# Performance work log

Measured on AMD Instinct MI355X. Metric: run time of the kernel, lower is better.

The kernel has to match this reference:

```python
import jax, jax.numpy as jnp
import numpy as np

EMBED_DIM = 1024
NUM_HEADS = 16
HEAD_DIM = EMBED_DIM // NUM_HEADS


def setup_inputs() -> dict:
    key = jax.random.key(0)
    ks = jax.random.split(key, 5)
    T, B, E = 2048, 2, EMBED_DIM
    s = 1.0 / np.sqrt(E)
    return {
        "x": jax.random.normal(ks[0], (T, B, E), jnp.float32),
        "wq": jax.random.normal(ks[1], (E, E), jnp.float32) * s,
        "bq": jnp.zeros((E,), jnp.float32),
        "wk": jax.random.normal(ks[2], (E, E), jnp.float32) * s,
        "bk": jnp.zeros((E,), jnp.float32),
        "wv": jax.random.normal(ks[3], (E, E), jnp.float32) * s,
        "bv": jnp.zeros((E,), jnp.float32),
        "wo": jax.random.normal(ks[4], (E, E), jnp.float32) * s,
        "bo": jnp.zeros((E,), jnp.float32),
    }


def reference(x, wq, bq, wk, bk, wv, bv, wo, bo):
    # x: [T, B, E] (Time x Batch x Channel), self-attention: query = key = value = x
    T, B, E = x.shape
    H, D = NUM_HEADS, HEAD_DIM
    scaling = D ** -0.5
    # Linear projections (torch Linear: y = x @ W.T + b)
    q = (jnp.einsum('tbe,fe->tbf', x, wq) + bq) * scaling
    k = jnp.einsum('tbe,fe->tbf', x, wk) + bk
    v = jnp.einsum('tbe,fe->tbf', x, wv) + bv
    # reshape to [B*H, T, D] equivalent -> use [B, H, T, D]
    q = q.reshape(T, B, H, D).transpose(1, 2, 0, 3)  # [B,H,T,D]
    k = k.reshape(T, B, H, D).transpose(1, 2, 0, 3)
    v = v.reshape(T, B, H, D).transpose(1, 2, 0, 3)
    # scores: [B,H,T,S], fp32 softmax
    scores = jnp.einsum('bhtd,bhsd->bhts', q, k)
    probs = jax.nn.softmax(scores.astype(jnp.float32), axis=-1).astype(x.dtype)
    attn = jnp.einsum('bhts,bhsd->bhtd', probs, v)  # [B,H,T,D]
    attn = attn.transpose(2, 0, 1, 3).reshape(T, B, E)
    out = jnp.einsum('tbe,fe->tbf', attn, wo) + bo
    return out
```

## Files before the change

### kernel.cpp

```cpp
#include <hip/hip_runtime.h>
#include <cstddef>
#include <cstdint>

#define T_DIM 2048
#define E_DIM 1024
#define M_DIM 4096

typedef __attribute__((ext_vector_type(8))) short short8;
typedef __attribute__((ext_vector_type(8))) _Float16 half8;
typedef __attribute__((ext_vector_type(4))) _Float16 half4;
typedef __attribute__((ext_vector_type(4))) float f32x4;

__device__ __forceinline__ short f16_bits(float v) {
  return __builtin_bit_cast(short, (_Float16)v);
}
__device__ __forceinline__ unsigned int pk2(float a, float b) {
  return __builtin_bit_cast(unsigned int, __builtin_amdgcn_cvt_pkrtz(a, b));
}
__device__ __forceinline__ half8 h8(short8 s) { return __builtin_bit_cast(half8, s); }

__device__ __forceinline__ void gl_lds16(const short* g, const short* l) {
  __builtin_amdgcn_global_load_lds(
      (const __attribute__((address_space(1))) unsigned int*)g,
      (__attribute__((address_space(3))) unsigned int*)l, 16, 0, 0);
}

__global__ __launch_bounds__(256) void convert_all(
    const float* __restrict__ x, const float* __restrict__ wq,
    const float* __restrict__ wk, const float* __restrict__ wv,
    const float* __restrict__ wo,
    short* __restrict__ xh, short* __restrict__ wqh, short* __restrict__ wkh,
    short* __restrict__ wvh, short* __restrict__ woh)
{
  const int bid = blockIdx.x;
  const float* in; short* hi; int base;
  if (bid < 4096)      { in = x;  hi = xh;  base = 0;    }
  else if (bid < 5120) { in = wq; hi = wqh; base = 4096; }
  else if (bid < 6144) { in = wk; hi = wkh; base = 5120; }
  else if (bid < 7168) { in = wv; hi = wvh; base = 6144; }
  else                 { in = wo; hi = woh; base = 7168; }
  const int i = (bid - base) * 256 + threadIdx.x;
  float4 v = ((const float4*)in)[i];
  uint2 p;
  p.x = (unsigned short)f16_bits(v.x) | ((unsigned int)(unsigned short)f16_bits(v.y) << 16);
  p.y = (unsigned short)f16_bits(v.z) | ((unsigned int)(unsigned short)f16_bits(v.w) << 16);
  ((uint2*)hi)[i] = p;
}

__global__ __launch_bounds__(256) void gemm_qkv(
    const short* __restrict__ xh,
    const short* __restrict__ wqh, const short* __restrict__ wkh,
    const short* __restrict__ wvh,
    const float* __restrict__ bq, const float* __restrict__ bk,
    const float* __restrict__ bv,
    short* __restrict__ qo, short* __restrict__ ko, short* __restrict__ vto)
{
  __shared__ __align__(16) short smem[128 * 64 * 2];
  short* Ah = smem;
  short* Wh = smem + 8192;
  const int tid = threadIdx.x;
  const int lane = tid & 63;
  const int w = tid >> 6;
  const int quad = lane >> 4;
  const int l15 = lane & 15;
  const int sel = blockIdx.x >> 3;
  const int n0 = (blockIdx.x & 7) * 128;
  const int m0 = blockIdx.y * 128;

  const short* wsel = sel == 0 ? wqh : sel == 1 ? wkh : wvh;
  const float* bias = sel == 0 ? bq : sel == 1 ? bk : bv;
  const float scale = sel == 0 ? 0.125f * 1.44269504088896f : 1.0f;

  const short* gsrc = (w < 2) ? xh : wsel;
  short* lbuf = (w < 2) ? Ah : Wh;
  const int rbase = (w < 2) ? m0 : n0;
  const int lrow8 = lane >> 3;
  const int gph8 = lane & 7;
  const int kg = (gph8 - lrow8) & 7;

  f32x4 zero = {0.f, 0.f, 0.f, 0.f};
  f32x4 acc[4][4];
#pragma unroll
  for (int i = 0; i < 4; ++i)
#pragma unroll
    for (int j = 0; j < 4; ++j) acc[i][j] = zero;

  const int wm = w & 1, wn = w >> 1;

  for (int k0 = 0; k0 < E_DIM; k0 += 64) {
    __syncthreads();
#pragma unroll
    for (int jj = 0; jj < 8; ++jj) {
      int j = (w & 1) * 8 + jj;
      int r = j * 8 + lrow8;
      gl_lds16(gsrc + (size_t)(rbase + r) * E_DIM + k0 + kg * 8, lbuf + j * 512);
    }
    __syncthreads();
#pragma unroll
    for (int ks = 0; ks < 2; ++ks) {
      short8 ahf[4];
#pragma unroll
      for (int i = 0; i < 4; ++i) {
        int r = wm * 64 + i * 16 + l15;
        ahf[i] = *(const short8*)&Ah[r * 64 + ((ks * 4 + quad + r) & 7) * 8];
      }
#pragma unroll
      for (int j = 0; j < 4; ++j) {
        int r = wn * 64 + j * 16 + l15;
        short8 bhf = *(const short8*)&Wh[r * 64 + ((ks * 4 + quad + r) & 7) * 8];
#pragma unroll
        for (int i = 0; i < 4; ++i)
          acc[i][j] = __builtin_amdgcn_mfma_f32_16x16x32_f16(h8(ahf[i]), h8(bhf), acc[i][j], 0, 0, 0);
      }
    }
  }

  if (sel < 2) {
#pragma unroll
    for (int j = 0; j < 4; ++j) {
      const int gc = n0 + wn * 64 + j * 16 + l15;
      const float bb = bias[gc];
      const int h = gc >> 6, d = gc & 63;
      short* dst = sel == 0 ? qo : ko;
#pragma unroll
      for (int i = 0; i < 4; ++i)
#pragma unroll
        for (int reg = 0; reg < 4; ++reg) {
          const int gm = m0 + wm * 64 + i * 16 + quad * 4 + reg;
          const float val = (acc[i][j][reg] + bb) * scale;
          const int t = gm >> 1, b = gm & 1;
          dst[((size_t)(b * 16 + h) * T_DIM + t) * 64 + d] = f16_bits(val);
        }
    }
  } else {
    short* Tb = smem;
    const int by = blockIdx.y;
#pragma unroll
    for (int R = 0; R < 2; ++R) {
      __syncthreads();
      if (wn == R) {
#pragma unroll
        for (int j = 0; j < 4; ++j) {
          const int nl = j * 16 + l15;
          const int gc = n0 + R * 64 + nl;
          const float bb = bias[gc];
#pragma unroll
          for (int i = 0; i < 4; ++i) {
            const int tp = wm * 32 + i * 8 + quad * 2;
            unsigned int lo = pk2(acc[i][j][0] + bb, acc[i][j][2] + bb);
            unsigned int hi = pk2(acc[i][j][1] + bb, acc[i][j][3] + bb);
            const int g0 = tp >> 3;
            const int sub = tp & 7;
            *(unsigned int*)&Tb[nl * 128 + ((g0 + nl) & 15) * 8 + sub] = lo;
            *(unsigned int*)&Tb[nl * 128 + ((g0 + 8 + nl) & 15) * 8 + sub] = hi;
          }
        }
      }
      __syncthreads();
#pragma unroll
      for (int ii = 0; ii < 4; ++ii) {
        const int n = w * 16 + ii * 4 + quad;
        const int g = (l15 - n) & 15;
        short8 vvec = *(const short8*)&Tb[n * 128 + l15 * 8];
        const int gc = n0 + R * 64 + n;
        const int h = gc >> 6, d = gc & 63;
        const int b = g >> 3;
        const int t = by * 64 + (g & 7) * 8;
        *(short8*)&vto[((size_t)(b * 16 + h) * 64 + d) * T_DIM + t] = vvec;
      }
    }
  }
}

__global__ __launch_bounds__(512, 4) void gemm_out_fused(
    const short* __restrict__ attn, const short* __restrict__ woh,
    const float* __restrict__ bo, float* __restrict__ out)
{
  __shared__ __align__(16) short smem[32768];
  const int tid = threadIdx.x;
  const int lane = tid & 63;
  const int w = tid >> 6;
  const int g = w >> 2;
  const int wg = w & 3;
  const int quad = lane >> 4;
  const int l15 = lane & 15;
  const int n0 = blockIdx.x * 128;
  const int m0 = blockIdx.y * 128;

  short* Ah = smem + g * 16384;
  short* Wh = Ah + 8192;
  const short* gsrc = (wg < 2) ? attn : woh;
  short* lbuf = (wg < 2) ? Ah : Wh;
  const int rbase = (wg < 2) ? m0 : n0;
  const int lrow8 = lane >> 3;
  const int gph8 = lane & 7;
  const int kg = (gph8 - lrow8) & 7;

  f32x4 zero = {0.f, 0.f, 0.f, 0.f};
  f32x4 acc[4][4];
#pragma unroll
  for (int i = 0; i < 4; ++i)
#pragma unroll
    for (int j = 0; j < 4; ++j) acc[i][j] = zero;

  const int wm = wg & 1, wn = wg >> 1;

  for (int k0 = g * 512; k0 < g * 512 + 512; k0 += 64) {
    __syncthreads();
#pragma unroll
    for (int jj = 0; jj < 8; ++jj) {
      int j = (wg & 1) * 8 + jj;
      int r = j * 8 + lrow8;
      gl_lds16(gsrc + (size_t)(rbase + r) * E_DIM + k0 + kg * 8, lbuf + j * 512);
    }
    __syncthreads();
#pragma unroll
    for (int ks = 0; ks < 2; ++ks) {
      short8 ahf[4];
#pragma unroll
      for (int i = 0; i < 4; ++i) {
        int r = wm * 64 + i * 16 + l15;
        ahf[i] = *(const short8*)&Ah[r * 64 + ((ks * 4 + quad + r) & 7) * 8];
      }
#pragma unroll
      for (int j = 0; j < 4; ++j) {
        int r = wn * 64 + j * 16 + l15;
        short8 bhf = *(const short8*)&Wh[r * 64 + ((ks * 4 + quad + r) & 7) * 8];
#pragma unroll
        for (int i = 0; i < 4; ++i)
          acc[i][j] = __builtin_amdgcn_mfma_f32_16x16x32_f16(h8(ahf[i]), h8(bhf), acc[i][j], 0, 0, 0);
      }
    }
  }

  __syncthreads();
  f32x4* Osc = (f32x4*)smem;
  if (g == 1) {
    f32x4* dst = Osc + wg * 1024;
#pragma unroll
    for (int i = 0; i < 4; ++i)
#pragma unroll
      for (int j = 0; j < 4; ++j)
        dst[(i * 4 + j) * 64 + lane] = acc[i][j];
  }
  __syncthreads();
  if (g == 0) {
    f32x4* src = Osc + wg * 1024;
#pragma unroll
    for (int j = 0; j < 4; ++j) {
      const int gc = n0 + wn * 64 + j * 16 + l15;
      const float bb = bo[gc];
#pragma unroll
      for (int i = 0; i < 4; ++i) {
        f32x4 t = src[(i * 4 + j) * 64 + lane];
#pragma unroll
        for (int reg = 0; reg < 4; ++reg) {
          const int gm = m0 + wm * 64 + i * 16 + quad * 4 + reg;
          out[(size_t)gm * E_DIM + gc] = acc[i][j][reg] + t[reg] + bb;
        }
      }
    }
  }
}

__global__ __launch_bounds__(256, 2) void attn_mfma(
    const short* __restrict__ q, const short* __restrict__ k,
    const short* __restrict__ vt, short* __restrict__ attn)
{
  __shared__ __align__(16) short SMEM[32768];
  __shared__ float l_red[4][128];
  short* Qs = SMEM;
  short* KV = SMEM + 8192;

  const int tid = threadIdx.x;
  const int lane = tid & 63;
  const int w = tid >> 6;
  const int quad = lane >> 4;
  const int l15 = lane & 15;
  const int bhid = blockIdx.y;
  const int b = bhid >> 4, h = bhid & 15;
  const int t0 = blockIdx.x * 128;

  const short* qb = q + (size_t)bhid * T_DIM * 64;
  const short* kb = k + (size_t)bhid * T_DIM * 64;
  const short* vb = vt + (size_t)bhid * 64 * T_DIM;

  const int lrow8 = lane >> 3;
  const int gph8 = lane & 7;

#pragma unroll
  for (int jj = 0; jj < 4; ++jj) {
    int j = w * 4 + jj;
    int r = j * 8 + lrow8;
    int gl = (gph8 - (r >> 1)) & 7;
    gl_lds16(qb + (size_t)(t0 + r) * 64 + gl * 8, Qs + j * 512);
  }

  const int kg = (gph8 - lrow8) & 7;
  const int vd = lane >> 1, vh = lane & 1;
#pragma unroll
  for (int c0 = 0; c0 < 2; ++c0) {
    short* slot = KV + c0 * 8192 + w * 2048;
    const int sg = c0 * 64 + w * 16;
    gl_lds16(kb + (size_t)(sg + lrow8) * 64 + kg * 8, slot);
    gl_lds16(kb + (size_t)(sg + lrow8 + 8) * 64 + kg * 8, slot + 512);
    gl_lds16(vb + (size_t)vd * T_DIM + sg + vh * 8, slot + 1024);
    gl_lds16(vb + (size_t)(vd + 32) * T_DIM + sg + vh * 8, slot + 1536);
  }
  __syncthreads();

  short8 qa[8][2];
#pragma unroll
  for (int qbk = 0; qbk < 8; ++qbk)
#pragma unroll
    for (int st = 0; st < 2; ++st) {
      int r = qbk * 16 + l15;
      int idx = r * 64 + (((st * 4 + quad) + (r >> 1)) & 7) * 8;
      qa[qbk][st] = *(const short8*)&Qs[idx];
    }

  f32x4 zero = {0.f, 0.f, 0.f, 0.f};
  f32x4 acc[4][8];
  float l_part[8];
#pragma unroll
  for (int d = 0; d < 4; ++d)
#pragma unroll
    for (int qb2 = 0; qb2 < 8; ++qb2) acc[d][qb2] = zero;
#pragma unroll
  for (int i = 0; i < 8; ++i) l_part[i] = 0.f;

  for (int c = 0; c < 32; ++c) {
    if (c >= 2) {
      if (c == 31) __builtin_amdgcn_s_waitcnt(0x0F70);
      else         __builtin_amdgcn_s_waitcnt(0x0F74);
    }
    const short* slot = KV + (c % 3) * 8192 + w * 2048;

    short8 kf[2];
#pragma unroll
    for (int st = 0; st < 2; ++st)
      kf[st] = *(const short8*)&slot[l15 * 64 + (((st * 4 + quad) + l15) & 7) * 8];
    uint2 vfu[4];
#pragma unroll
    for (int dblk = 0; dblk < 4; ++dblk)
      vfu[dblk] = *(const uint2*)&slot[1024 + (dblk * 16 + l15) * 16 + quad * 4];

    if (c < 30) {
      short* nslot = KV + ((c + 2) % 3) * 8192 + w * 2048;
      const int sg = (c + 2) * 64 + w * 16;
      gl_lds16(kb + (size_t)(sg + lrow8) * 64 + kg * 8, nslot);
      gl_lds16(kb + (size_t)(sg + lrow8 + 8) * 64 + kg * 8, nslot + 512);
      gl_lds16(vb + (size_t)vd * T_DIM + sg + vh * 8, nslot + 1024);
      gl_lds16(vb + (size_t)(vd + 32) * T_DIM + sg + vh * 8, nslot + 1536);
    }

    uint2 pb[8];
#pragma unroll
    for (int qbk = 0; qbk < 8; ++qbk) {
      f32x4 s = zero;
      s = __builtin_amdgcn_mfma_f32_16x16x32_f16(h8(kf[0]), h8(qa[qbk][0]), s, 0, 0, 0);
      s = __builtin_amdgcn_mfma_f32_16x16x32_f16(h8(kf[1]), h8(qa[qbk][1]), s, 0, 0, 0);
      float p0 = __builtin_amdgcn_exp2f(s[0]);
      float p1 = __builtin_amdgcn_exp2f(s[1]);
      float p2 = __builtin_amdgcn_exp2f(s[2]);
      float p3 = __builtin_amdgcn_exp2f(s[3]);
      l_part[qbk] += (p0 + p1) + (p2 + p3);
      pb[qbk].x = pk2(p0, p1);
      pb[qbk].y = pk2(p2, p3);
    }

#pragma unroll
    for (int dblk = 0; dblk < 4; ++dblk) {
      half4 va = __builtin_bit_cast(half4, vfu[dblk]);
#pragma unroll
      for (int qbk = 0; qbk < 8; ++qbk)
        acc[dblk][qbk] = __builtin_amdgcn_mfma_f32_16x16x16f16(
            va, __builtin_bit_cast(half4, pb[qbk]), acc[dblk][qbk], 0, 0, 0);
    }
  }

#pragma unroll
  for (int qbk = 0; qbk < 8; ++qbk) {
    float l = l_part[qbk];
    l += __shfl_xor(l, 16);
    l += __shfl_xor(l, 32);
    if (quad == 0) l_red[w][qbk * 16 + l15] = l;
  }

  f32x4* Osc = (f32x4*)SMEM;
  __syncthreads();
  if (w & 1) {
    f32x4* dst = Osc + (w >> 1) * 2048;
#pragma unroll
    for (int dblk = 0; dblk < 4; ++dblk)
#pragma unroll
      for (int qbk = 0; qbk < 8; ++qbk)
        dst[(dblk * 8 + qbk) * 64 + lane] = acc[dblk][qbk];
  }
  __syncthreads();
  if (!(w & 1)) {
    f32x4* src = Osc + (w >> 1) * 2048;
#pragma unroll
    for (int dblk = 0; dblk < 4; ++dblk)
#pragma unroll
      for (int qbk = 0; qbk < 8; ++qbk) {
        f32x4 t = src[(dblk * 8 + qbk) * 64 + lane];
        acc[dblk][qbk][0] += t[0]; acc[dblk][qbk][1] += t[1];
        acc[dblk][qbk][2] += t[2]; acc[dblk][qbk][3] += t[3];
      }
  }
  __syncthreads();
  if (w == 2) {
#pragma unroll
    for (int d2 = 0; d2 < 2; ++d2)
#pragma unroll
      for (int qbk = 0; qbk < 8; ++qbk)
        Osc[(d2 * 8 + qbk) * 64 + lane] = acc[d2][qbk];
  }
  if (w == 0) {
#pragma unroll
    for (int d2 = 0; d2 < 2; ++d2)
#pragma unroll
      for (int qbk = 0; qbk < 8; ++qbk)
        Osc[1024 + (d2 * 8 + qbk) * 64 + lane] = acc[2 + d2][qbk];
  }
  __syncthreads();
  if (w == 0) {
#pragma unroll
    for (int qbk = 0; qbk < 8; ++qbk) {
      const int qq = qbk * 16 + l15;
      const float lsum = l_red[0][qq] + l_red[1][qq] + l_red[2][qq] + l_red[3][qq];
      const float inv = 1.f / lsum;
      const int t = t0 + qq;
      const size_t mrow = (size_t)(t * 2 + b) * E_DIM;
#pragma unroll
      for (int d2 = 0; d2 < 2; ++d2) {
        f32x4 t4 = Osc[(d2 * 8 + qbk) * 64 + lane];
        uint2 ov;
        ov.x = pk2((acc[d2][qbk][0] + t4[0]) * inv, (acc[d2][qbk][1] + t4[1]) * inv);
        ov.y = pk2((acc[d2][qbk][2] + t4[2]) * inv, (acc[d2][qbk][3] + t4[3]) * inv);
        *(uint2*)&attn[mrow + h * 64 + d2 * 16 + quad * 4] = ov;
      }
    }
  }
  if (w == 2) {
#pragma unroll
    for (int qbk = 0; qbk < 8; ++qbk) {
      const int qq = qbk * 16 + l15;
      const float lsum = l_red[0][qq] + l_red[1][qq] + l_red[2][qq] + l_red[3][qq];
      const float inv = 1.f / lsum;
      const int t = t0 + qq;
      const size_t mrow = (size_t)(t * 2 + b) * E_DIM;
#pragma unroll
      for (int d2 = 0; d2 < 2; ++d2) {
        f32x4 t4 = Osc[1024 + (d2 * 8 + qbk) * 64 + lane];
        uint2 ov;
        ov.x = pk2((acc[2 + d2][qbk][0] + t4[0]) * inv, (acc[2 + d2][qbk][1] + t4[1]) * inv);
        ov.y = pk2((acc[2 + d2][qbk][2] + t4[2]) * inv, (acc[2 + d2][qbk][3] + t4[3]) * inv);
        *(uint2*)&attn[mrow + h * 64 + (2 + d2) * 16 + quad * 4] = ov;
      }
    }
  }
}

extern "C" void kernel_launch(void* const* d_in, const int* in_sizes, int n_in,
                              void* d_out, int out_size, void* d_ws, size_t ws_size,
                              hipStream_t stream)
{
  const float* x  = (const float*)d_in[0];
  const float* wq = (const float*)d_in[1];
  const float* bq = (const float*)d_in[2];
  const float* wk = (const float*)d_in[3];
  const float* bk = (const float*)d_in[4];
  const float* wv = (const float*)d_in[5];
  const float* bv = (const float*)d_in[6];
  const float* wo = (const float*)d_in[7];
  const float* bo = (const float*)d_in[8];
  float* out = (float*)d_out;

  short* ws = (short*)d_ws;
  const size_t M4 = (size_t)M_DIM * E_DIM;
  const size_t M1 = (size_t)E_DIM * E_DIM;
  short* aws  = ws;
  short* woh  = aws + M4;
  short* xh   = woh + M1;
  short* wqh  = xh + M4;
  short* wkh  = wqh + M1;
  short* wvh  = wkh + M1;
  short* qws  = wvh + M1;
  short* kws  = qws + M4;
  short* vtws = kws + M4;

  convert_all<<<8192, 256, 0, stream>>>(x, wq, wk, wv, wo, xh, wqh, wkh, wvh, woh);
  gemm_qkv<<<dim3(24, 32), 256, 0, stream>>>(xh, wqh, wkh, wvh, bq, bk, bv,
                                             qws, kws, vtws);
  attn_mfma<<<dim3(16, 32), 256, 0, stream>>>(qws, kws, vtws, aws);
  gemm_out_fused<<<dim3(8, 32), 512, 0, stream>>>(aws, woh, bo, out);
}
```

Measured before the change: 193.5 us.

## Deepen attention K/V prefetch to three stages with register double-buffering

Restructures the attention main loop so K/V tiles are prefetched three chunks ahead instead of two. Fragments for the next chunk are read from LDS into a second register set while MFMAs run on the current one, with the loop unrolled by two to ping-pong the buffers. It also raises wave priority around the MFMA section and remaps block indices so consecutive blocks cover different heads. The aim is to hide global and LDS latency behind compute, at the cost of more registers and occupancy risk under the 2-wave launch bound.

```diff
diff --git a/kernel.cpp b/kernel.cpp
--- a/kernel.cpp
+++ b/kernel.cpp
@@ -263,6 +263,63 @@
   }
 }
 
+__device__ __forceinline__ void attn_step(
+    int c, const short* KV, int w, const short* kb, const short* vb,
+    int lrow8, int kg, int vd, int vh, int quad, int l15,
+    short8 (&kcur)[2], uint2 (&vcur)[4],
+    short8 (&knxt)[2], uint2 (&vnxt)[4],
+    const short8 (&qa)[8][2], f32x4 (&acc)[4][8], float (&l_part)[8])
+{
+  const f32x4 zero = {0.f, 0.f, 0.f, 0.f};
+
+  if (c < 29) {
+    __builtin_amdgcn_s_waitcnt(0xC07F);
+    const short* fs = KV + (c % 3) * 8192 + w * 2048;
+    const int sg = (c + 3) * 64 + w * 16;
+    gl_lds16(kb + (size_t)(sg + lrow8) * 64 + kg * 8, fs);
+    gl_lds16(kb + (size_t)(sg + lrow8 + 8) * 64 + kg * 8, fs + 512);
+    gl_lds16(vb + (size_t)vd * T_DIM + sg + vh * 8, fs + 1024);
+    gl_lds16(vb + (size_t)(vd + 32) * T_DIM + sg + vh * 8, fs + 1536);
+  }
+
+  if (c < 31) {
+    if (c < 29)       __builtin_amdgcn_s_waitcnt(0x0F78);
+    else if (c == 29) __builtin_amdgcn_s_waitcnt(0x0F74);
+    else              __builtin_amdgcn_s_waitcnt(0x0F70);
+    const short* ns = KV + ((c + 1) % 3) * 8192 + w * 2048;
+    knxt[0] = *(const short8*)&ns[l15 * 64 + ((quad + l15) & 7) * 8];
+    knxt[1] = *(const short8*)&ns[l15 * 64 + ((4 + quad + l15) & 7) * 8];
+#pragma unroll
+    for (int dblk = 0; dblk < 4; ++dblk)
+      vnxt[dblk] = *(const uint2*)&ns[1024 + (dblk * 16 + l15) * 16 + quad * 4];
+  }
+
+  __builtin_amdgcn_s_setprio(1);
+  uint2 pb[8];
+#pragma unroll
+  for (int qbk = 0; qbk < 8; ++qbk) {
+    f32x4 s = zero;
+    s = __builtin_amdgcn_mfma_f32_16x16x32_f16(h8(kcur[0]), h8(qa[qbk][0]), s, 0, 0, 0);
+    s = __builtin_amdgcn_mfma_f32_16x16x32_f16(h8(kcur[1]), h8(qa[qbk][1]), s, 0, 0, 0);
+    float p0 = __builtin_amdgcn_exp2f(s[0]);
+    float p1 = __builtin_amdgcn_exp2f(s[1]);
+    float p2 = __builtin_amdgcn_exp2f(s[2]);
+    float p3 = __builtin_amdgcn_exp2f(s[3]);
+    l_part[qbk] += (p0 + p1) + (p2 + p3);
+    pb[qbk].x = pk2(p0, p1);
+    pb[qbk].y = pk2(p2, p3);
+  }
+#pragma unroll
+  for (int dblk = 0; dblk < 4; ++dblk) {
+    half4 va = __builtin_bit_cast(half4, vcur[dblk]);
+#pragma unroll
+    for (int qbk = 0; qbk < 8; ++qbk)
+      acc[dblk][qbk] = __builtin_amdgcn_mfma_f32_16x16x16f16(
+          va, __builtin_bit_cast(half4, pb[qbk]), acc[dblk][qbk], 0, 0, 0);
+  }
+  __builtin_amdgcn_s_setprio(0);
+}
+
 __global__ __launch_bounds__(256, 2) void attn_mfma(
     const short* __restrict__ q, const short* __restrict__ k,
     const short* __restrict__ vt, short* __restrict__ attn)
@@ -277,9 +334,11 @@
   const int w = tid >> 6;
   const int quad = lane >> 4;
   const int l15 = lane & 15;
-  const int bhid = blockIdx.y;
+
+  const int fid = blockIdx.y * 16 + blockIdx.x;
+  const int bhid = fid & 31;
+  const int t0 = (fid >> 5) * 128;
   const int b = bhid >> 4, h = bhid & 15;
-  const int t0 = blockIdx.x * 128;
 
   const short* qb = q + (size_t)bhid * T_DIM * 64;
   const short* kb = k + (size_t)bhid * T_DIM * 64;
@@ -299,7 +358,7 @@
   const int kg = (gph8 - lrow8) & 7;
   const int vd = lane >> 1, vh = lane & 1;
 #pragma unroll
-  for (int c0 = 0; c0 < 2; ++c0) {
+  for (int c0 = 0; c0 < 3; ++c0) {
     short* slot = KV + c0 * 8192 + w * 2048;
     const int sg = c0 * 64 + w * 16;
     gl_lds16(kb + (size_t)(sg + lrow8) * 64 + kg * 8, slot);
@@ -329,54 +388,22 @@
 #pragma unroll
   for (int i = 0; i < 8; ++i) l_part[i] = 0.f;
 
-  for (int c = 0; c < 32; ++c) {
-    if (c >= 2) {
-      if (c == 31) __builtin_amdgcn_s_waitcnt(0x0F70);
-      else         __builtin_amdgcn_s_waitcnt(0x0F74);
-    }
-    const short* slot = KV + (c % 3) * 8192 + w * 2048;
-
-    short8 kf[2];
-#pragma unroll
-    for (int st = 0; st < 2; ++st)
-      kf[st] = *(const short8*)&slot[l15 * 64 + (((st * 4 + quad) + l15) & 7) * 8];
-    uint2 vfu[4];
+  short8 kfA[2], kfB[2];
+  uint2 vfA[4], vfB[4];
+  {
+    const short* ns = KV + w * 2048;
+    kfA[0] = *(const short8*)&ns[l15 * 64 + ((quad + l15) & 7) * 8];
+    kfA[1] = *(const short8*)&ns[l15 * 64 + ((4 + quad + l15) & 7) * 8];
 #pragma unroll
     for (int dblk = 0; dblk < 4; ++dblk)
-      vfu[dblk] = *(const uint2*)&slot[1024 + (dblk * 16 + l15) * 16 + quad * 4];
-
-    if (c < 30) {
-      short* nslot = KV + ((c + 2) % 3) * 8192 + w * 2048;
-      const int sg = (c + 2) * 64 + w * 16;
-      gl_lds16(kb + (size_t)(sg + lrow8) * 64 + kg * 8, nslot);
-      gl_lds16(kb + (size_t)(sg + lrow8 + 8) * 64 + kg * 8, nslot + 512);
-      gl_lds16(vb + (size_t)vd * T_DIM + sg + vh * 8, nslot + 1024);
-      gl_lds16(vb + (size_t)(vd + 32) * T_DIM + sg + vh * 8, nslot + 1536);
-    }
-
-    uint2 pb[8];
-#pragma unroll
-    for (int qbk = 0; qbk < 8; ++qbk) {
-      f32x4 s = zero;
-      s = __builtin_amdgcn_mfma_f32_16x16x32_f16(h8(kf[0]), h8(qa[qbk][0]), s, 0, 0, 0);
-      s = __builtin_amdgcn_mfma_f32_16x16x32_f16(h8(kf[1]), h8(qa[qbk][1]), s, 0, 0, 0);
-      float p0 = __builtin_amdgcn_exp2f(s[0]);
-      float p1 = __builtin_amdgcn_exp2f(s[1]);
-      float p2 = __builtin_amdgcn_exp2f(s[2]);
-      float p3 = __builtin_amdgcn_exp2f(s[3]);
-      l_part[qbk] += (p0 + p1) + (p2 + p3);
-      pb[qbk].x = pk2(p0, p1);
-      pb[qbk].y = pk2(p2, p3);
-    }
-
-#pragma unroll
-    for (int dblk = 0; dblk < 4; ++dblk) {
-      half4 va = __builtin_bit_cast(half4, vfu[dblk]);
-#pragma unroll
-      for (int qbk = 0; qbk < 8; ++qbk)
-        acc[dblk][qbk] = __builtin_amdgcn_mfma_f32_16x16x16f16(
-            va, __builtin_bit_cast(half4, pb[qbk]), acc[dblk][qbk], 0, 0, 0);
-    }
+      vfA[dblk] = *(const uint2*)&ns[1024 + (dblk * 16 + l15) * 16 + quad * 4];
+  }
+
+  for (int c = 0; c < 32; c += 2) {
+    attn_step(c,     KV, w, kb, vb, lrow8, kg, vd, vh, quad, l15,
+              kfA, vfA, kfB, vfB, qa, acc, l_part);
+    attn_step(c + 1, KV, w, kb, vb, lrow8, kg, vd, vh, quad, l15,
+              kfB, vfB, kfA, vfA, qa, acc, l_part);
   }
 
 #pragma unroll
```

Measured after the change: 243.7 us. +25.9%, slower.
